# Optimization experiments

Measured on AMD Instinct MI355X. Metric: run time of the kernel, lower is better.

## Reference

```python
import jax, jax.numpy as jnp
import numpy as np

N_NODES = 100000
N_EDGES = 3200000
NUM_GRAPHS = 64
NEG_SLOPE = 0.2  # PyG GATConv default leaky_relu slope


def gat_conv(x, src, dst, W, att_src, att_dst, bias, heads, out_ch, concat):
    """PyG GATConv (default args: add_self_loops=True, negative_slope=0.2).
    src/dst already include self loops."""
    n = x.shape[0]
    h = (x @ W).reshape(n, heads, out_ch)              # [N,H,C]
    a_src = jnp.sum(h * att_src, axis=-1)              # [N,H]
    a_dst = jnp.sum(h * att_dst, axis=-1)              # [N,H]
    e = jax.nn.leaky_relu(a_src[src] + a_dst[dst], NEG_SLOPE)  # [E,H]
    # segment softmax over destination nodes
    m = jax.ops.segment_max(e, dst, num_segments=n)
    ex = jnp.exp(e - m[dst])
    denom = jax.ops.segment_sum(ex, dst, num_segments=n)
    alpha = ex / (denom[dst] + 1e-16)                  # [E,H]
    msg = h[src] * alpha[:, :, None]                   # [E,H,C]
    out = jax.ops.segment_sum(msg, dst, num_segments=n)  # [N,H,C]
    if concat:
        out = out.reshape(n, heads * out_ch)
    else:
        out = out.mean(axis=1)
    return out + bias


def setup_inputs() -> dict:
    key = jax.random.key(0)
    ks = jax.random.split(key, 12)
    x = jax.random.normal(ks[0], (N_NODES, 4), dtype=jnp.float32)
    edge_index = jax.random.randint(ks[1], (2, N_EDGES), 0, N_NODES, dtype=jnp.int64)
    batch = jnp.sort(jax.random.randint(ks[2], (N_NODES,), 0, NUM_GRAPHS, dtype=jnp.int64))
    s = 0.1
    return {
        "x": x,
        "edge_index": edge_index,
        "batch": batch,
        "W1": jax.random.normal(ks[3], (4, 64), dtype=jnp.float32) * s,
        "att_src1": jax.random.normal(ks[4], (2, 32), dtype=jnp.float32) * s,
        "att_dst1": jax.random.normal(ks[5], (2, 32), dtype=jnp.float32) * s,
        "bias1": jnp.zeros((64,), dtype=jnp.float32),
        "W2": jax.random.normal(ks[6], (64, 64), dtype=jnp.float32) * s,
        "att_src2": jax.random.normal(ks[7], (1, 64), dtype=jnp.float32) * s,
        "att_dst2": jax.random.normal(ks[8], (1, 64), dtype=jnp.float32) * s,
        "bias2": jnp.zeros((64,), dtype=jnp.float32),
    }


def reference(x, edge_index, batch, W1, att_src1, att_dst1, bias1, W2, att_src2, att_dst2, bias2):
    n = x.shape[0]
    loops = jnp.arange(n, dtype=edge_index.dtype)
    src = jnp.concatenate([edge_index[0], loops])
    dst = jnp.concatenate([edge_index[1], loops])
    h = gat_conv(x, src, dst, W1, att_src1, att_dst1, bias1, heads=2, out_ch=32, concat=True)
    h = jax.nn.elu(h)
    # dropout is identity in eval mode
    h = gat_conv(h, src, dst, W2, att_src2, att_dst2, bias2, heads=1, out_ch=64, concat=False)
    # global_mean_pool
    sums = jax.ops.segment_sum(h, batch, num_segments=NUM_GRAPHS)
    counts = jax.ops.segment_sum(jnp.ones((n,), h.dtype), batch, num_segments=NUM_GRAPHS)
    return sums / jnp.maximum(counts, 1.0)[:, None]
```

## Files before the change

kernel.cpp:

```cpp
#include <hip/hip_runtime.h>
#include <hip/hip_bf16.h>
#include <hip/hip_fp16.h>
#include <math.h>


__device__ __forceinline__ float leaky(float x) { return x >= 0.f ? x : 0.2f * x; }
__device__ __forceinline__ int iclamp(int v, int lo, int hi) {
  return v < lo ? lo : (v > hi ? hi : v);
}
__device__ __forceinline__ unsigned char f8(float v) {
  return (unsigned char)(__builtin_amdgcn_cvt_pk_fp8_f32(v, v, 0, false) & 0xff);
}
__device__ __forceinline__ float hlo(unsigned w) {
  __half2 h = *(__half2*)&w; return __half2float(h.x);
}
__device__ __forceinline__ float hhi(unsigned w) {
  __half2 h = *(__half2*)&w; return __half2float(h.y);
}

typedef __attribute__((ext_vector_type(8))) _Float16 f16x8;
typedef __attribute__((ext_vector_type(4))) float f32x4;
typedef __attribute__((ext_vector_type(2))) float f32x2;

#define NBUCK 1024
#define BSHIFT 7
#define BCAP 4608
#define CSRSZ (NBUCK * BCAP)
#define MAXR 8
#define SCAP (MAXR * 1024)

__global__ __launch_bounds__(1024, 8) void k_scatt(
    const int* __restrict__ ei, int E, int n, int* __restrict__ bcur,
    unsigned* __restrict__ pairs,
    const float* __restrict__ x, const float* __restrict__ W1,
    const float* __restrict__ att_src1, const float* __restrict__ att_dst1,
    uint4* __restrict__ xs, float* __restrict__ a_dst1, int NBK) {
  __shared__ int h[NBUCK];
  __shared__ int cur[NBUCK];
  __shared__ int gofs[NBUCK];
  __shared__ int wtot[16];
  __shared__ int htot;
  __shared__ unsigned sstage[SCAP];
  __shared__ unsigned short sbkt[SCAP];
  __shared__ float W1s[256];
  __shared__ float as1[64];
  __shared__ float ad1[64];
  int t = threadIdx.x;
  if (blockIdx.x >= NBK) {
    if (t < 256) W1s[t] = W1[t];
    else if (t >= 256 && t < 320) as1[t - 256] = att_src1[t - 256];
    else if (t >= 320 && t < 384) ad1[t - 320] = att_dst1[t - 320];
    __syncthreads();
    int grp = t >> 4, sub = t & 15;
    int node = (blockIdx.x - NBK) * 64 + grp;
    if (node >= n) return;
    float4 xr = ((const float4*)x)[node];
    float vs = 0.f, vd = 0.f;
    #pragma unroll
    for (int i = 0; i < 4; ++i) {
      int c = sub * 4 + i;
      float hv = xr.x * W1s[c] + xr.y * W1s[64 + c] + xr.z * W1s[128 + c] + xr.w * W1s[192 + c];
      vs = fmaf(hv, as1[c], vs);
      vd = fmaf(hv, ad1[c], vd);
    }
    #pragma unroll
    for (int m = 4; m >= 1; m >>= 1) { vs += __shfl_xor(vs, m); vd += __shfl_xor(vd, m); }
    int wl = t & 63;
    float vs1 = __shfl(vs, (wl & 48) + 8);
    float vd1 = __shfl(vd, (wl & 48) + 8);
    if (sub == 0) {
      __half2 x01 = __float22half2_rn(make_float2(xr.x, xr.y));
      __half2 x23 = __float22half2_rn(make_float2(xr.z, xr.w));
      uint4 rec;
      rec.x = *(unsigned*)&x01;
      rec.y = *(unsigned*)&x23;
      rec.z = __float_as_uint(vs);
      rec.w = __float_as_uint(vs1);
      xs[node] = rec;
      ((float2*)a_dst1)[node] = make_float2(vd, vd1);
    }
    return;
  }
  h[t] = 0;
  __syncthreads();
  int chunk = (E + NBK - 1) / NBK;
  chunk = (chunk + 1) & ~1;
  int beg = blockIdx.x * chunk;
  int end = beg + chunk; if (end > E) end = E;
  unsigned pR[MAXR];
  unsigned short bR[MAXR];
  int cntr = 0;
  for (int i = beg + 2 * t; i < end && cntr < MAXR; i += 2048) {
    if (i + 1 < end) {
      int2 sv = *(const int2*)(ei + i);
      int2 dv = *(const int2*)(ei + E + i);
      {
        int s = iclamp(sv.x, 0, n - 1);
        int d = iclamp(dv.x, 0, n - 1);
        int bkt = d >> BSHIFT;
        pR[cntr] = ((unsigned)(d & 127) << 25) | (unsigned)s;
        bR[cntr] = (unsigned short)bkt;
        atomicAdd(&h[bkt], 1);
        ++cntr;
      }
      if (cntr < MAXR) {
        int s = iclamp(sv.y, 0, n - 1);
        int d = iclamp(dv.y, 0, n - 1);
        int bkt = d >> BSHIFT;
        pR[cntr] = ((unsigned)(d & 127) << 25) | (unsigned)s;
        bR[cntr] = (unsigned short)bkt;
        atomicAdd(&h[bkt], 1);
        ++cntr;
      }
    } else {
      int s = iclamp(ei[i], 0, n - 1);
      int d = iclamp(ei[E + i], 0, n - 1);
      int bkt = d >> BSHIFT;
      pR[cntr] = ((unsigned)(d & 127) << 25) | (unsigned)s;
      bR[cntr] = (unsigned short)bkt;
      atomicAdd(&h[bkt], 1);
      ++cntr;
    }
  }
  __syncthreads();
  int v = h[t];
  int lanei = t & 63, wid = t >> 6;
  int sc = v;
  #pragma unroll
  for (int ofs = 1; ofs < 64; ofs <<= 1) {
    int u = __shfl_up(sc, ofs);
    if (lanei >= ofs) sc += u;
  }
  if (lanei == 63) wtot[wid] = sc;
  __syncthreads();
  if (wid == 0 && lanei < 16) {
    int wv = wtot[lanei];
    int s2 = wv;
    #pragma unroll
    for (int ofs = 1; ofs < 16; ofs <<= 1) {
      int u = __shfl_up(s2, ofs);
      if (lanei >= ofs) s2 += u;
    }
    wtot[lanei] = s2 - wv;
  }
  __syncthreads();
  int incl = sc + wtot[wid];
  int loff = incl - v;
  cur[t] = loff;
  gofs[t] = t * BCAP + (v ? atomicAdd(&bcur[t], v) : 0) - loff;
  if (t == 1023) htot = incl;
  __syncthreads();
  for (int k = 0; k < cntr; ++k) {
    int b = bR[k];
    int lpos = atomicAdd(&cur[b], 1);
    sstage[lpos] = pR[k];
    sbkt[lpos] = (unsigned short)b;
  }
  __syncthreads();
  int total = htot;
  for (int i = t; i < total; i += 1024) {
    int b = sbkt[i];
    int pos = gofs[b] + i;
    if (pos >= b * BCAP && pos < (b + 1) * BCAP) pairs[pos] = sstage[i];
  }
}

__global__ __launch_bounds__(256) void k_bgat1(
    const unsigned* __restrict__ pairs, const int* __restrict__ bcur,
    const uint4* __restrict__ xs, const float* __restrict__ W1,
    const float* __restrict__ a_dst1, const float* __restrict__ bias1,
    int* __restrict__ rowbeg, int* __restrict__ rowend, int* __restrict__ csr,
    __half* __restrict__ hB, int n) {
  __shared__ int lcsr[BCAP];
  __shared__ int praw[BCAP];
  __shared__ int sh[128];
  __shared__ int cur[128];
  __shared__ int lrb[128];
  __shared__ int lre[128];
  __shared__ int wt[2];
  __shared__ float W1s[256];
  int t = threadIdx.x;
  W1s[t] = W1[t];
  int b = blockIdx.x;
  int node0 = b << BSHIFT;
  if (node0 >= n) return;
  int base = b * BCAP;
  int cnt = iclamp(bcur[b], 0, BCAP);
  if (t < 128) sh[t] = 0;
  __syncthreads();
  for (int i = t; i < cnt; i += 256) {
    int pv = (int)pairs[base + i];
    praw[i] = pv;
    atomicAdd(&sh[((unsigned)pv) >> 25], 1);
  }
  __syncthreads();
  int v = (t < 128) ? sh[t] : 0;
  int lanei = t & 63, wid = t >> 6;
  int sc = v;
  if (wid < 2) {
    #pragma unroll
    for (int ofs = 1; ofs < 64; ofs <<= 1) {
      int u = __shfl_up(sc, ofs);
      if (lanei >= ofs) sc += u;
    }
    if (lanei == 63) wt[wid] = sc;
  }
  __syncthreads();
  if (t < 128) {
    int off = sc + ((wid == 1) ? wt[0] : 0) - v;
    cur[t] = off;
    lrb[t] = off;
    lre[t] = off + v;
    int node = node0 + t;
    if (node < n) {
      rowbeg[node] = base + off;
      rowend[node] = base + off + v;
    }
  }
  __syncthreads();
  for (int i = t; i < cnt; i += 256) {
    unsigned p = (unsigned)praw[i];
    int l = p >> 25;
    int r = atomicAdd(&cur[l], 1);
    if (r >= 0 && r < BCAP) lcsr[r] = (int)(p & 0x1ffffffu);
  }
  __syncthreads();
  for (int i = t; i < cnt; i += 256)
    csr[base + i] = lcsr[i];
  int wave = t >> 6, lane = t & 63;
  int nd = (lane >> 4), sub = lane & 15;
  for (int rnd = 0; rnd < 8; ++rnd) {
    int nodeLocal = rnd * 16 + wave * 4 + nd;
    int node = node0 + nodeLocal;
    bool valid = node < n;
    int nc = valid ? node : 0;
    int ebeg = valid ? lrb[nodeLocal] : 0;
    int eend = valid ? lre[nodeLocal] : 0;
    ebeg = iclamp(ebeg, 0, BCAP);
    eend = iclamp(eend, ebeg, BCAP);
    float2 ad = ((const float2*)a_dst1)[nc];
    uint4 rs = xs[nc];
    float A0 = 0.f, A1 = 0.f, A2 = 0.f, A3 = 0.f, dn0 = 0.f;
    float B0 = 0.f, B1 = 0.f, B2 = 0.f, B3 = 0.f, dn1 = 0.f;
    int e = ebeg + sub;
    for (; e + 16 < eend; e += 32) {
      int sa = iclamp(lcsr[e], 0, n - 1);
      int sb = iclamp(lcsr[e + 16], 0, n - 1);
      uint4 ra = xs[sa];
      uint4 rb = xs[sb];
      float ea0 = __expf(leaky(__uint_as_float(ra.z) + ad.x));
      float ea1 = __expf(leaky(__uint_as_float(ra.w) + ad.y));
      float eb0 = __expf(leaky(__uint_as_float(rb.z) + ad.x));
      float eb1 = __expf(leaky(__uint_as_float(rb.w) + ad.y));
      dn0 += ea0 + eb0; dn1 += ea1 + eb1;
      float xa0 = hlo(ra.x), xa1 = hhi(ra.x), xa2 = hlo(ra.y), xa3 = hhi(ra.y);
      float xb0 = hlo(rb.x), xb1 = hhi(rb.x), xb2 = hlo(rb.y), xb3 = hhi(rb.y);
      A0 = fmaf(ea0, xa0, A0); A1 = fmaf(ea0, xa1, A1);
      A2 = fmaf(ea0, xa2, A2); A3 = fmaf(ea0, xa3, A3);
      B0 = fmaf(ea1, xa0, B0); B1 = fmaf(ea1, xa1, B1);
      B2 = fmaf(ea1, xa2, B2); B3 = fmaf(ea1, xa3, B3);
      A0 = fmaf(eb0, xb0, A0); A1 = fmaf(eb0, xb1, A1);
      A2 = fmaf(eb0, xb2, A2); A3 = fmaf(eb0, xb3, A3);
      B0 = fmaf(eb1, xb0, B0); B1 = fmaf(eb1, xb1, B1);
      B2 = fmaf(eb1, xb2, B2); B3 = fmaf(eb1, xb3, B3);
    }
    if (e < eend) {
      int s = iclamp(lcsr[e], 0, n - 1);
      uint4 rr = xs[s];
      float ex0 = __expf(leaky(__uint_as_float(rr.z) + ad.x));
      float ex1 = __expf(leaky(__uint_as_float(rr.w) + ad.y));
      dn0 += ex0; dn1 += ex1;
      float x0 = hlo(rr.x), x1 = hhi(rr.x), x2 = hlo(rr.y), x3 = hhi(rr.y);
      A0 = fmaf(ex0, x0, A0); A1 = fmaf(ex0, x1, A1);
      A2 = fmaf(ex0, x2, A2); A3 = fmaf(ex0, x3, A3);
      B0 = fmaf(ex1, x0, B0); B1 = fmaf(ex1, x1, B1);
      B2 = fmaf(ex1, x2, B2); B3 = fmaf(ex1, x3, B3);
    }
    bool lo = (sub < 8);
    float C0, C1, C2, C3, dnC, sA, sB;
    sA = __shfl_xor(A0, 8); sB = __shfl_xor(B0, 8); C0 = lo ? A0 + sA : B0 + sB;
    sA = __shfl_xor(A1, 8); sB = __shfl_xor(B1, 8); C1 = lo ? A1 + sA : B1 + sB;
    sA = __shfl_xor(A2, 8); sB = __shfl_xor(B2, 8); C2 = lo ? A2 + sA : B2 + sB;
    sA = __shfl_xor(A3, 8); sB = __shfl_xor(B3, 8); C3 = lo ? A3 + sA : B3 + sB;
    sA = __shfl_xor(dn0, 8); sB = __shfl_xor(dn1, 8); dnC = lo ? dn0 + sA : dn1 + sB;
    #pragma unroll
    for (int m = 4; m >= 1; m >>= 1) {
      C0 += __shfl_xor(C0, m); C1 += __shfl_xor(C1, m);
      C2 += __shfl_xor(C2, m); C3 += __shfl_xor(C3, m);
      dnC += __shfl_xor(dnC, m);
    }
    float exs = __expf(leaky(__uint_as_float(lo ? rs.z : rs.w) + (lo ? ad.x : ad.y)));
    dnC += exs;
    float xs0 = hlo(rs.x), xs1 = hhi(rs.x), xs2 = hlo(rs.y), xs3 = hhi(rs.y);
    C0 = fmaf(exs, xs0, C0); C1 = fmaf(exs, xs1, C1);
    C2 = fmaf(exs, xs2, C2); C3 = fmaf(exs, xs3, C3);
    float inv = 1.0f / (dnC + 1e-16f);
    if (valid) {
      int f0 = sub * 4;
      float vv[4];
      #pragma unroll
      for (int i = 0; i < 4; ++i) {
        int f = f0 + i;
        float accv = C0 * W1s[f] + C1 * W1s[64 + f] + C2 * W1s[128 + f] + C3 * W1s[192 + f];
        float vx = accv * inv + bias1[f];
        vv[i] = vx > 0.f ? vx : expm1f(vx);
      }
      __half2 h01 = __float22half2_rn(make_float2(vv[0], vv[1]));
      __half2 h23 = __float22half2_rn(make_float2(vv[2], vv[3]));
      uint2 pk;
      pk.x = *(unsigned*)&h01;
      pk.y = *(unsigned*)&h23;
      *(uint2*)(hB + (size_t)node * 64 + f0) = pk;
    }
  }
}

__global__ __launch_bounds__(256) void k_lin2(
    const __half* __restrict__ hB, const float* __restrict__ W2,
    const float* __restrict__ att_src2, const float* __restrict__ att_dst2,
    float* __restrict__ a_src2, float* __restrict__ a_dst2,
    unsigned char* __restrict__ hC, int n) {
  __shared__ __attribute__((aligned(16))) _Float16 Whi[64 * 72];
  __shared__ __attribute__((aligned(16))) _Float16 Wlo[64 * 72];
  int t = threadIdx.x;
  for (int i = t; i < 4096; i += 256) {
    int k = i >> 6, col = i & 63;
    float w = W2[i];
    _Float16 hi = (_Float16)w;
    _Float16 lo = (_Float16)(w - (float)hi);
    Whi[col * 72 + k] = hi;
    Wlo[col * 72 + k] = lo;
  }
  __syncthreads();
  int wave = t >> 6, lane = t & 63;
  int quad = lane >> 4, c = lane & 15;
  float as2[4], ad2[4];
  #pragma unroll
  for (int tt = 0; tt < 4; ++tt) {
    as2[tt] = att_src2[tt * 16 + c];
    ad2[tt] = att_dst2[tt * 16 + c];
  }
  for (int it = 0; it < 4; ++it) {
    int m0 = blockIdx.x * 256 + wave * 64 + it * 16;
    if (m0 >= n) break;
    int mrow = m0 + c; if (mrow > n - 1) mrow = n - 1;
    const _Float16* hrow = (const _Float16*)(hB + (size_t)mrow * 64);
    f16x8 a0 = *(const f16x8*)(hrow + quad * 8);
    f16x8 a1 = *(const f16x8*)(hrow + 32 + quad * 8);
    f32x4 zero = {0.f, 0.f, 0.f, 0.f};
    f32x4 acc[4] = {zero, zero, zero, zero};
    #pragma unroll
    for (int tt = 0; tt < 4; ++tt) {
      int nn = tt * 16 + c;
      const _Float16* wh = &Whi[nn * 72];
      const _Float16* wl = &Wlo[nn * 72];
      f16x8 bh0 = *(const f16x8*)(wh + quad * 8);
      f16x8 bh1 = *(const f16x8*)(wh + 32 + quad * 8);
      f16x8 bl0 = *(const f16x8*)(wl + quad * 8);
      f16x8 bl1 = *(const f16x8*)(wl + 32 + quad * 8);
      acc[tt] = __builtin_amdgcn_mfma_f32_16x16x32_f16(a0, bh0, acc[tt], 0, 0, 0);
      acc[tt] = __builtin_amdgcn_mfma_f32_16x16x32_f16(a1, bh1, acc[tt], 0, 0, 0);
      acc[tt] = __builtin_amdgcn_mfma_f32_16x16x32_f16(a0, bl0, acc[tt], 0, 0, 0);
      acc[tt] = __builtin_amdgcn_mfma_f32_16x16x32_f16(a1, bl1, acc[tt], 0, 0, 0);
    }
    #pragma unroll
    for (int r = 0; r < 4; ++r) {
      float s = 0.f, d = 0.f;
      #pragma unroll
      for (int tt = 0; tt < 4; ++tt) {
        s = fmaf(acc[tt][r], as2[tt], s);
        d = fmaf(acc[tt][r], ad2[tt], d);
      }
      #pragma unroll
      for (int msk = 8; msk >= 1; msk >>= 1) {
        s += __shfl_xor(s, msk);
        d += __shfl_xor(d, msk);
      }
      int m = m0 + quad * 4 + r;
      if (m < n) {
        if (c == 0) { a_src2[m] = s; a_dst2[m] = d; }
        unsigned char* orow = hC + (size_t)m * 64;
        #pragma unroll
        for (int tt = 0; tt < 4; ++tt)
          orow[tt * 16 + c] = f8(acc[tt][r]);
      }
    }
  }
}

#define ACC8(HW, EE) do { \
    f32x2 _a = __builtin_amdgcn_cvt_pk_f32_fp8((HW).x, false); \
    f32x2 _b = __builtin_amdgcn_cvt_pk_f32_fp8((HW).x, true); \
    ac0 = fmaf((EE), _a.x, ac0); ac1 = fmaf((EE), _a.y, ac1); \
    ac2 = fmaf((EE), _b.x, ac2); ac3 = fmaf((EE), _b.y, ac3); \
    _a = __builtin_amdgcn_cvt_pk_f32_fp8((HW).y, false); \
    _b = __builtin_amdgcn_cvt_pk_f32_fp8((HW).y, true); \
    ac4 = fmaf((EE), _a.x, ac4); ac5 = fmaf((EE), _a.y, ac5); \
    ac6 = fmaf((EE), _b.x, ac6); ac7 = fmaf((EE), _b.y, ac7); \
  } while (0)

__global__ __launch_bounds__(256) void k_gat2(
    const unsigned char* __restrict__ hC, const float* __restrict__ a_src2,
    const float* __restrict__ a_dst2, const int* __restrict__ rowbeg,
    const int* __restrict__ rowend, const int* __restrict__ csr,
    const float* __restrict__ bias2,
    __half* __restrict__ h2, int n, int node0) {
  __shared__ unsigned long long stage[4 * 64];
  int t = threadIdx.x;
  int w = t >> 6, lane = t & 63;
  int node = node0 + blockIdx.x * 4 + w;
  if (node >= n) return;
  int beg = iclamp(rowbeg[node], 0, CSRSZ);
  int end = iclamp(rowend[node], beg, CSRSZ);
  float ad = a_dst2[node];
  int g = lane >> 3;
  int p = lane & 7;
  const uint2* hrows = (const uint2*)hC;
  unsigned long long* st = &stage[w * 64];
  float ac0 = 0.f, ac1 = 0.f, ac2 = 0.f, ac3 = 0.f;
  float ac4 = 0.f, ac5 = 0.f, ac6 = 0.f, ac7 = 0.f;
  float dn = 0.f;
  for (int tb = beg; tb < end; tb += 64) {
    int tc = end - tb; if (tc > 64) tc = 64;
    int s = 0; float ex = 0.f;
    if (lane < tc) {
      s = iclamp(csr[tb + lane], 0, n - 1);
      ex = __expf(leaky(a_src2[s] + ad));
    }
    dn += ex;
    st[lane] = ((unsigned long long)(unsigned)s << 32) | (unsigned)__float_as_uint(ex);
    int steps = (tc + 7) >> 3;
    int j = 0;
    for (; j + 4 <= steps; j += 4) {
      unsigned long long pk0 = st[(j + 0) * 8 + g];
      unsigned long long pk1 = st[(j + 1) * 8 + g];
      unsigned long long pk2 = st[(j + 2) * 8 + g];
      unsigned long long pk3 = st[(j + 3) * 8 + g];
      int s0 = (int)(pk0 >> 32), s1 = (int)(pk1 >> 32);
      int s2 = (int)(pk2 >> 32), s3 = (int)(pk3 >> 32);
      float e0 = __uint_as_float((unsigned)pk0);
      float e1 = __uint_as_float((unsigned)pk1);
      float e2 = __uint_as_float((unsigned)pk2);
      float e3 = __uint_as_float((unsigned)pk3);
      uint2 hw0 = hrows[(size_t)s0 * 8 + p];
      uint2 hw1 = hrows[(size_t)s1 * 8 + p];
      uint2 hw2 = hrows[(size_t)s2 * 8 + p];
      uint2 hw3 = hrows[(size_t)s3 * 8 + p];
      ACC8(hw0, e0);
      ACC8(hw1, e1);
      ACC8(hw2, e2);
      ACC8(hw3, e3);
    }
    for (; j < steps; ++j) {
      unsigned long long pk0 = st[j * 8 + g];
      int s0 = (int)(pk0 >> 32);
      float e0 = __uint_as_float((unsigned)pk0);
      uint2 hw0 = hrows[(size_t)s0 * 8 + p];
      ACC8(hw0, e0);
    }
  }
  #pragma unroll
  for (int m = 8; m <= 32; m <<= 1) {
    ac0 += __shfl_xor(ac0, m); ac1 += __shfl_xor(ac1, m);
    ac2 += __shfl_xor(ac2, m); ac3 += __shfl_xor(ac3, m);
    ac4 += __shfl_xor(ac4, m); ac5 += __shfl_xor(ac5, m);
    ac6 += __shfl_xor(ac6, m); ac7 += __shfl_xor(ac7, m);
  }
  #pragma unroll
  for (int m = 32; m >= 1; m >>= 1) dn += __shfl_xor(dn, m);
  float exs = __expf(leaky(a_src2[node] + ad));
  dn += exs;
  uint2 hs = hrows[(size_t)node * 8 + p];
  ACC8(hs, exs);
  if (g == 0) {
    float inv = 1.0f / (dn + 1e-16f);
    const float* b2 = bias2 + p * 8;
    __half2 o0 = __float22half2_rn(make_float2(ac0 * inv + b2[0], ac1 * inv + b2[1]));
    __half2 o1 = __float22half2_rn(make_float2(ac2 * inv + b2[2], ac3 * inv + b2[3]));
    __half2 o2 = __float22half2_rn(make_float2(ac4 * inv + b2[4], ac5 * inv + b2[5]));
    __half2 o3 = __float22half2_rn(make_float2(ac6 * inv + b2[6], ac7 * inv + b2[7]));
    uint4 pk;
    pk.x = *(unsigned*)&o0; pk.y = *(unsigned*)&o1;
    pk.z = *(unsigned*)&o2; pk.w = *(unsigned*)&o3;
    ((uint4*)(h2 + (size_t)node * 64))[p] = pk;
  }
}

__global__ __launch_bounds__(256) void k_pool(
    const __half* __restrict__ h2, const int* __restrict__ batch,
    float* __restrict__ pool, float* __restrict__ cnt, int n, int G) {
  const int PW = 64;
  int wave = blockIdx.x * 4 + (threadIdx.x >> 6);
  int lane = threadIdx.x & 63;
  int start = wave * PW;
  if (start < n) {
    int end = start + PW; if (end > n) end = n;
    int bcur = iclamp(batch[start], 0, G - 1);
    float acc = 0.f, count = 0.f;
    for (int i = start; i < end; ++i) {
      int b = iclamp(batch[i], 0, G - 1);
      if (b != bcur) {
        atomicAdd(&pool[bcur * 64 + lane], acc);
        if (lane == 0) atomicAdd(&cnt[bcur], count);
        bcur = b; acc = 0.f; count = 0.f;
      }
      acc += __half2float(h2[(size_t)i * 64 + lane]);
      count += 1.f;
    }
    atomicAdd(&pool[bcur * 64 + lane], acc);
    if (lane == 0) atomicAdd(&cnt[bcur], count);
  }
}

__global__ void k_final(const float* __restrict__ pool, const float* __restrict__ cnt,
                        float* __restrict__ out, int G) {
  int i = blockIdx.x * blockDim.x + threadIdx.x;
  if (i >= G * 64) return;
  out[i] = pool[i] / fmaxf(cnt[i >> 6], 1.0f);
}

extern "C" void kernel_launch(void* const* d_in, const int* in_sizes, int n_in,
                              void* d_out, int out_size, void* d_ws, size_t ws_size,
                              hipStream_t stream) {
  const float* x        = (const float*)d_in[0];
  const int*   ei       = (const int*)d_in[1];
  const int*   batch    = (const int*)d_in[2];
  const float* W1       = (const float*)d_in[3];
  const float* att_src1 = (const float*)d_in[4];
  const float* att_dst1 = (const float*)d_in[5];
  const float* bias1    = (const float*)d_in[6];
  const float* W2       = (const float*)d_in[7];
  const float* att_src2 = (const float*)d_in[8];
  const float* att_dst2 = (const float*)d_in[9];
  const float* bias2    = (const float*)d_in[10];

  const int n = in_sizes[0] / 4;
  const int E = in_sizes[1] / 2;
  const int G = out_size / 64;

  char* p = (char*)d_ws;
  auto alloc = [&](size_t bytes) -> void* {
    void* r = (void*)p;
    p += (bytes + 255) & ~(size_t)255;
    return r;
  };
  unsigned* pairs = (unsigned*)alloc((size_t)CSRSZ * 4);
  int* csr = (int*)pairs;
  size_t hsz = (size_t)n * 64 * 2;
  char* R = (char*)alloc(hsz + (size_t)n * 64);
  __half* hB = (__half*)R;
  __half* h2 = (__half*)R;
  unsigned char* hC = (unsigned char*)(R + hsz);
  uint4* xs     = (uint4*)alloc((size_t)n * 16);
  int*   rowbeg = (int*)alloc((size_t)n * 4);
  int*   rowend = (int*)alloc((size_t)n * 4);
  size_t poolelems = (size_t)G * 64 + G;
  char*  Z = (char*)alloc(poolelems * 4 + (size_t)NBUCK * 4);
  float* pool = (float*)Z;
  float* cnt  = pool + (size_t)G * 64;
  int*   bcur = (int*)(Z + poolelems * 4);
  float* a_dst1 = (float*)alloc((size_t)n * 2 * 4);
  float* a_src2 = (float*)alloc((size_t)n * 4);
  float* a_dst2 = (float*)alloc((size_t)n * 4);

  hipMemsetAsync(Z, 0, poolelems * 4 + (size_t)NBUCK * 4, stream);

  int NBK = (E + MAXR * 1024 - 1) / (MAXR * 1024);
  if (NBK < 512) NBK = 512;
  int natt = (n + 63) / 64;

  k_scatt<<<NBK + natt, 1024, 0, stream>>>(ei, E, n, bcur, pairs,
                                           x, W1, att_src1, att_dst1, xs, a_dst1, NBK);
  k_bgat1<<<NBUCK, 256, 0, stream>>>(pairs, bcur, xs, W1, a_dst1, bias1,
                                     rowbeg, rowend, csr, hB, n);
  k_lin2<<<(n + 255) / 256, 256, 0, stream>>>(hB, W2, att_src2, att_dst2, a_src2, a_dst2, hC, n);
  int nh = ((n / 2) + 3) & ~3;
  if (nh > n) nh = n;
  k_gat2<<<(nh + 3) / 4, 256, 0, stream>>>(hC, a_src2, a_dst2, rowbeg, rowend, csr, bias2, h2, n, 0);
  if (n > nh)
    k_gat2<<<(n - nh + 3) / 4, 256, 0, stream>>>(hC, a_src2, a_dst2, rowbeg, rowend, csr, bias2, h2, n, nh);
  k_pool<<<(n + 255) / 256, 256, 0, stream>>>(h2, batch, pool, cnt, n, G);
  k_final<<<(G * 64 + 255) / 256, 256, 0, stream>>>(pool, cnt, (float*)d_out, G);
}
```

Before: 248.1 us.

## Split layer-2 fp8 features into two 32-column planes and aggregate per plane

```diff
diff --git a/kernel.cpp b/kernel.cpp
--- a/kernel.cpp
+++ b/kernel.cpp
@@ -340,6 +340,7 @@
     as2[tt] = att_src2[tt * 16 + c];
     ad2[tt] = att_dst2[tt * 16 + c];
   }
+  size_t plane = (size_t)n * 32;
   for (int it = 0; it < 4; ++it) {
     int m0 = blockIdx.x * 256 + wave * 64 + it * 16;
     if (m0 >= n) break;
@@ -379,10 +380,12 @@
       int m = m0 + quad * 4 + r;
       if (m < n) {
         if (c == 0) { a_src2[m] = s; a_dst2[m] = d; }
-        unsigned char* orow = hC + (size_t)m * 64;
-        #pragma unroll
-        for (int tt = 0; tt < 4; ++tt)
-          orow[tt * 16 + c] = f8(acc[tt][r]);
+        unsigned char* r0 = hC + (size_t)m * 32;
+        unsigned char* r1 = hC + plane + (size_t)m * 32;
+        r0[c]      = f8(acc[0][r]);
+        r0[16 + c] = f8(acc[1][r]);
+        r1[c]      = f8(acc[2][r]);
+        r1[16 + c] = f8(acc[3][r]);
       }
     }
   }
@@ -404,85 +407,81 @@
     const float* __restrict__ a_dst2, const int* __restrict__ rowbeg,
     const int* __restrict__ rowend, const int* __restrict__ csr,
     const float* __restrict__ bias2,
-    __half* __restrict__ h2, int n, int node0) {
+    __half* __restrict__ h2, int n) {
   __shared__ unsigned long long stage[4 * 64];
   int t = threadIdx.x;
   int w = t >> 6, lane = t & 63;
-  int node = node0 + blockIdx.x * 4 + w;
+  int node = blockIdx.x * 4 + w;
   if (node >= n) return;
   int beg = iclamp(rowbeg[node], 0, CSRSZ);
   int end = iclamp(rowend[node], beg, CSRSZ);
   float ad = a_dst2[node];
-  int g = lane >> 3;
-  int p = lane & 7;
-  const uint2* hrows = (const uint2*)hC;
+  float asn = a_src2[node];
+  int gg = lane >> 2;
+  int pp = lane & 3;
+  size_t plane = (size_t)n * 32;
   unsigned long long* st = &stage[w * 64];
-  float ac0 = 0.f, ac1 = 0.f, ac2 = 0.f, ac3 = 0.f;
-  float ac4 = 0.f, ac5 = 0.f, ac6 = 0.f, ac7 = 0.f;
   float dn = 0.f;
-  for (int tb = beg; tb < end; tb += 64) {
-    int tc = end - tb; if (tc > 64) tc = 64;
-    int s = 0; float ex = 0.f;
-    if (lane < tc) {
-      s = iclamp(csr[tb + lane], 0, n - 1);
-      ex = __expf(leaky(a_src2[s] + ad));
-    }
-    dn += ex;
-    st[lane] = ((unsigned long long)(unsigned)s << 32) | (unsigned)__float_as_uint(ex);
-    int steps = (tc + 7) >> 3;
-    int j = 0;
-    for (; j + 4 <= steps; j += 4) {
-      unsigned long long pk0 = st[(j + 0) * 8 + g];
-      unsigned long long pk1 = st[(j + 1) * 8 + g];
-      unsigned long long pk2 = st[(j + 2) * 8 + g];
-      unsigned long long pk3 = st[(j + 3) * 8 + g];
-      int s0 = (int)(pk0 >> 32), s1 = (int)(pk1 >> 32);
-      int s2 = (int)(pk2 >> 32), s3 = (int)(pk3 >> 32);
-      float e0 = __uint_as_float((unsigned)pk0);
-      float e1 = __uint_as_float((unsigned)pk1);
-      float e2 = __uint_as_float((unsigned)pk2);
-      float e3 = __uint_as_float((unsigned)pk3);
-      uint2 hw0 = hrows[(size_t)s0 * 8 + p];
-      uint2 hw1 = hrows[(size_t)s1 * 8 + p];
-      uint2 hw2 = hrows[(size_t)s2 * 8 + p];
-      uint2 hw3 = hrows[(size_t)s3 * 8 + p];
+  float inv = 0.f;
+  #pragma unroll
+  for (int hh = 0; hh < 2; ++hh) {
+    const uint2* hr = (const uint2*)(hC + (size_t)hh * plane);
+    float ac0 = 0.f, ac1 = 0.f, ac2 = 0.f, ac3 = 0.f;
+    float ac4 = 0.f, ac5 = 0.f, ac6 = 0.f, ac7 = 0.f;
+    for (int tb = beg; tb < end; tb += 64) {
+      int tc = end - tb; if (tc > 64) tc = 64;
+      int s = 0; float ex = 0.f;
+      if (lane < tc) {
+        s = iclamp(csr[tb + lane], 0, n - 1);
+        ex = __expf(leaky(a_src2[s] + ad));
+      }
+      if (hh == 0) dn += ex;
+      st[lane] = ((unsigned long long)(unsigned)s << 32) | (unsigned)__float_as_uint(ex);
+      int steps = (tc + 15) >> 4;
+      uint2 hw0, hw1, hw2, hw3;
+      float e0, e1, e2, e3;
+#define GLD(J, HW, EE) { \
+      unsigned long long pk = st[(J) * 16 + gg]; \
+      int ss = (int)(pk >> 32); \
+      EE = __uint_as_float((unsigned)pk); \
+      HW = hr[(size_t)ss * 4 + pp]; }
+      GLD(0, hw0, e0);
+      if (steps > 1) GLD(1, hw1, e1);
+      if (steps > 2) GLD(2, hw2, e2);
+      if (steps > 3) GLD(3, hw3, e3);
+#undef GLD
       ACC8(hw0, e0);
-      ACC8(hw1, e1);
-      ACC8(hw2, e2);
-      ACC8(hw3, e3);
-    }
-    for (; j < steps; ++j) {
-      unsigned long long pk0 = st[j * 8 + g];
-      int s0 = (int)(pk0 >> 32);
-      float e0 = __uint_as_float((unsigned)pk0);
-      uint2 hw0 = hrows[(size_t)s0 * 8 + p];
-      ACC8(hw0, e0);
-    }
-  }
-  #pragma unroll
-  for (int m = 8; m <= 32; m <<= 1) {
-    ac0 += __shfl_xor(ac0, m); ac1 += __shfl_xor(ac1, m);
-    ac2 += __shfl_xor(ac2, m); ac3 += __shfl_xor(ac3, m);
-    ac4 += __shfl_xor(ac4, m); ac5 += __shfl_xor(ac5, m);
-    ac6 += __shfl_xor(ac6, m); ac7 += __shfl_xor(ac7, m);
-  }
-  #pragma unroll
-  for (int m = 32; m >= 1; m >>= 1) dn += __shfl_xor(dn, m);
-  float exs = __expf(leaky(a_src2[node] + ad));
-  dn += exs;
-  uint2 hs = hrows[(size_t)node * 8 + p];
-  ACC8(hs, exs);
-  if (g == 0) {
-    float inv = 1.0f / (dn + 1e-16f);
-    const float* b2 = bias2 + p * 8;
-    __half2 o0 = __float22half2_rn(make_float2(ac0 * inv + b2[0], ac1 * inv + b2[1]));
-    __half2 o1 = __float22half2_rn(make_float2(ac2 * inv + b2[2], ac3 * inv + b2[3]));
-    __half2 o2 = __float22half2_rn(make_float2(ac4 * inv + b2[4], ac5 * inv + b2[5]));
-    __half2 o3 = __float22half2_rn(make_float2(ac6 * inv + b2[6], ac7 * inv + b2[7]));
-    uint4 pk;
-    pk.x = *(unsigned*)&o0; pk.y = *(unsigned*)&o1;
-    pk.z = *(unsigned*)&o2; pk.w = *(unsigned*)&o3;
-    ((uint4*)(h2 + (size_t)node * 64))[p] = pk;
+      if (steps > 1) ACC8(hw1, e1);
+      if (steps > 2) ACC8(hw2, e2);
+      if (steps > 3) ACC8(hw3, e3);
+    }
+    #pragma unroll
+    for (int m = 4; m <= 32; m <<= 1) {
+      ac0 += __shfl_xor(ac0, m); ac1 += __shfl_xor(ac1, m);
+      ac2 += __shfl_xor(ac2, m); ac3 += __shfl_xor(ac3, m);
+      ac4 += __shfl_xor(ac4, m); ac5 += __shfl_xor(ac5, m);
+      ac6 += __shfl_xor(ac6, m); ac7 += __shfl_xor(ac7, m);
+    }
+    float exs = __expf(leaky(asn + ad));
+    if (hh == 0) {
+      #pragma unroll
+      for (int m = 32; m >= 1; m >>= 1) dn += __shfl_xor(dn, m);
+      dn += exs;
+      inv = 1.0f / (dn + 1e-16f);
+    }
+    uint2 hs = hr[(size_t)node * 4 + pp];
+    ACC8(hs, exs);
+    if (gg == 0) {
+      const float* b2 = bias2 + hh * 32 + pp * 8;
+      __half2 o0 = __float22half2_rn(make_float2(ac0 * inv + b2[0], ac1 * inv + b2[1]));
+      __half2 o1 = __float22half2_rn(make_float2(ac2 * inv + b2[2], ac3 * inv + b2[3]));
+      __half2 o2 = __float22half2_rn(make_float2(ac4 * inv + b2[4], ac5 * inv + b2[5]));
+      __half2 o3 = __float22half2_rn(make_float2(ac6 * inv + b2[6], ac7 * inv + b2[7]));
+      uint4 pk;
+      pk.x = *(unsigned*)&o0; pk.y = *(unsigned*)&o1;
+      pk.z = *(unsigned*)&o2; pk.w = *(unsigned*)&o3;
+      ((uint4*)(h2 + (size_t)node * 64 + hh * 32))[pp] = pk;
+    }
   }
 }
 
@@ -574,11 +573,7 @@
   k_bgat1<<<NBUCK, 256, 0, stream>>>(pairs, bcur, xs, W1, a_dst1, bias1,
                                      rowbeg, rowend, csr, hB, n);
   k_lin2<<<(n + 255) / 256, 256, 0, stream>>>(hB, W2, att_src2, att_dst2, a_src2, a_dst2, hC, n);
-  int nh = ((n / 2) + 3) & ~3;
-  if (nh > n) nh = n;
-  k_gat2<<<(nh + 3) / 4, 256, 0, stream>>>(hC, a_src2, a_dst2, rowbeg, rowend, csr, bias2, h2, n, 0);
-  if (n > nh)
-    k_gat2<<<(n - nh + 3) / 4, 256, 0, stream>>>(hC, a_src2, a_dst2, rowbeg, rowend, csr, bias2, h2, n, nh);
+  k_gat2<<<(n + 3) / 4, 256, 0, stream>>>(hC, a_src2, a_dst2, rowbeg, rowend, csr, bias2, h2, n);
   k_pool<<<(n + 255) / 256, 256, 0, stream>>>(h2, batch, pool, cnt, n, G);
   k_final<<<(G * 64 + 255) / 256, 256, 0, stream>>>(pool, cnt, (float*)d_out, G);
 }
```

New measurement: 283.5 us. 1.14x slower.
